# Performance work log

Measured on AMD Instinct MI355X. Metric: run time of the kernel, lower is better.

Reference implementation:

```python
import jax, jax.numpy as jnp
import numpy as np

B, NS, NC = 4096, 1024, 256
GUMBEL_HARD = True


def _linear(x, W, b):
    # torch nn.Linear: y = x @ W.T + b, W is [out, in]
    return x @ W.T + b


def _gumbel_softmax(logits, gnoise, tau, hard):
    y = jax.nn.softmax((logits + gnoise) / tau, axis=-1)
    if hard:
        y_hard = jax.nn.one_hot(jnp.argmax(y, axis=-1), y.shape[-1], dtype=y.dtype)
        y = y_hard + y - jax.lax.stop_gradient(y)  # straight-through
    return y


def setup_inputs() -> dict:
    key = jax.random.key(0)
    ks = jax.random.split(key, 32)
    inp = {
        "ct": jax.random.normal(ks[0], (B, NC), jnp.float32),
        "b1": jax.random.uniform(ks[1], (B, 2), jnp.float32),
        "b2": jax.random.uniform(ks[2], (B, 2), jnp.float32),
        "b3": jax.random.uniform(ks[3], (B, 2), jnp.float32),
        "rnn1": jax.random.normal(ks[4], (B, NS), jnp.float32),
        "rnn2": jax.random.normal(ks[5], (B, NS), jnp.float32),
        "rnn3": jax.random.normal(ks[6], (B, NS), jnp.float32),
        "rnn4": jax.random.normal(ks[7], (B, NS), jnp.float32),
        "gn1": jax.random.gumbel(ks[8], (B, 2), jnp.float32),
        "gn2": jax.random.gumbel(ks[9], (B, 2), jnp.float32),
        "gn3": jax.random.gumbel(ks[10], (B, 2), jnp.float32),
        "theta": 1,
    }
    def lin(k, out_d, in_d):
        return (0.02 * jax.random.normal(k, (out_d, in_d), jnp.float32),
                jnp.zeros((out_d,), jnp.float32))
    shapes = {
        "e_ct": (NS, NC), "rnn1_b0": (NS, 2 * NS), "rnn1_b1": (NS, 2 * NS),
        "b1_rnn1": (2, NS), "rnn2_b0": (NS, 2 * NS), "rnn2_b1": (NS, 2 * NS),
        "b2_rnn2": (2, NS), "rnn3_b0": (NS, 2 * NS), "rnn3_b1": (NS, 2 * NS),
        "b3_rnn3": (2, NS), "rnn4": (NS, 2 * NS), "hg_rnns": (NS, 4 * NS),
        "g_hg": (4, NS), "hctpi_rnns": (NS, 4 * NS), "ctpi_hctpi": (NC, NS),
    }
    for i, (name, (o, ii)) in enumerate(shapes.items()):
        W, bb = lin(ks[11 + i], o, ii)
        inp["W_" + name] = W
        inp["b_" + name] = bb
    return inp


def reference(ct, b1, b2, b3, rnn1, rnn2, rnn3, rnn4, gn1, gn2, gn3, theta,
              W_e_ct, b_e_ct, W_rnn1_b0, b_rnn1_b0, W_rnn1_b1, b_rnn1_b1,
              W_b1_rnn1, b_b1_rnn1, W_rnn2_b0, b_rnn2_b0, W_rnn2_b1, b_rnn2_b1,
              W_b2_rnn2, b_b2_rnn2, W_rnn3_b0, b_rnn3_b0, W_rnn3_b1, b_rnn3_b1,
              W_b3_rnn3, b_b3_rnn3, W_rnn4, b_rnn4, W_hg_rnns, b_hg_rnns,
              W_g_hg, b_g_hg, W_hctpi_rnns, b_hctpi_rnns, W_ctpi_hctpi, b_ctpi_hctpi):
    tau = jnp.float32(theta)
    b1tm1f = b1[:, 0:1]
    ct_e = jax.nn.relu(_linear(ct, W_e_ct, b_e_ct))

    rnn1b1 = jnp.tanh(_linear(jnp.concatenate((rnn2, ct_e), axis=1), W_rnn1_b1, b_rnn1_b1))
    rnn1b0 = jnp.tanh(_linear(jnp.concatenate((rnn1, ct_e), axis=1), W_rnn1_b0, b_rnn1_b0))
    rnn1t = b1tm1f * rnn1b1 + (1.0 - b1tm1f) * rnn1b0
    b1t = _gumbel_softmax(_linear(rnn1t, W_b1_rnn1, b_b1_rnn1), gn1, tau, GUMBEL_HARD)
    b1tf = b1t[:, 0:1]

    b2tm1f = b2[:, 0:1]
    rnn2b1 = jnp.tanh(_linear(jnp.concatenate((rnn3, rnn1t), axis=1), W_rnn2_b1, b_rnn2_b1))
    rnn2b0 = jnp.tanh(_linear(jnp.concatenate((rnn2, rnn1t), axis=1), W_rnn2_b0, b_rnn2_b0))
    rnn2_inner = (1.0 - b2tm1f) * rnn2b0 + b2tm1f * rnn2b1
    rnn2t = (1.0 - b1tf) * rnn2 + b1tf * rnn2_inner
    b2tnew = _gumbel_softmax(_linear(rnn2t, W_b2_rnn2, b_b2_rnn2), gn2, tau, GUMBEL_HARD)
    b2t = b1tf * b2tnew + (1.0 - b1tf) * b2
    b2tf = b2t[:, 0:1]

    b3tm1f = b3[:, 0:1]
    rnn3b1 = jnp.tanh(_linear(jnp.concatenate((rnn4, rnn2t), axis=1), W_rnn3_b1, b_rnn3_b1))
    rnn3b0 = jnp.tanh(_linear(jnp.concatenate((rnn3, rnn2t), axis=1), W_rnn3_b0, b_rnn3_b0))
    rnn3_inner = b3tm1f * rnn3b1 + (1.0 - b3tm1f) * rnn3b0
    rnn3t = (1.0 - b1tf) * rnn3 + b1tf * ((1.0 - b2tf) * rnn3 + b2tf * rnn3_inner)
    b3tnew = _gumbel_softmax(_linear(rnn3t, W_b3_rnn3, b_b3_rnn3), gn3, tau, GUMBEL_HARD)
    b3t = b1tf * (b2tf * b3tnew + (1.0 - b2tf) * b3) + (1.0 - b1tf) * b3
    b3tf = b3t[:, 0:1]

    rnn4_inner = jnp.tanh(_linear(jnp.concatenate((rnn4, rnn3t), axis=1), W_rnn4, b_rnn4))
    rnn4t = (1.0 - b1tf) * rnn4 + b1tf * ((1.0 - b2tf) * rnn4 + b2tf * ((1.0 - b3tf) * rnn4 + b3tf * rnn4_inner))

    hg = jax.nn.relu(_linear(jnp.concatenate((rnn1t, rnn2t, rnn3t, rnn4t), axis=1), W_hg_rnns, b_hg_rnns))
    g = jax.nn.sigmoid(_linear(hg, W_g_hg, b_g_hg))
    gated = jnp.concatenate((g[:, 0:1] * rnn1t, g[:, 1:2] * rnn2t, g[:, 2:3] * rnn3t, g[:, 3:4] * rnn4t), axis=1)
    hctpi = jax.nn.relu(_linear(gated, W_hctpi_rnns, b_hctpi_rnns))
    ctpi = jax.nn.log_softmax(_linear(hctpi, W_ctpi_hctpi, b_ctpi_hctpi), axis=1)
    return (ctpi, b1t, b2t, b3t, rnn1t, rnn2t, rnn3t, rnn4t)
```

## Files before the change

### kernel.cpp

```cpp
#include <hip/hip_runtime.h>
#include <cstdint>
#include <cstddef>

typedef unsigned short u16;
typedef __bf16 bf16x8 __attribute__((ext_vector_type(8)));
typedef float  f32x4  __attribute__((ext_vector_type(4)));
typedef u16    u16x4  __attribute__((ext_vector_type(4)));

__device__ __forceinline__ void splitv(const float4 a, const float4 b, bf16x8& h, bf16x8& l) {
    float x[8] = {a.x, a.y, a.z, a.w, b.x, b.y, b.z, b.w};
#pragma unroll
    for (int i = 0; i < 8; i++) {
        __bf16 hh = (__bf16)x[i];
        h[i] = hh;
        l[i] = (__bf16)(x[i] - (float)hh);
    }
}
__device__ __forceinline__ void hiv(const float4 a, const float4 b, bf16x8& h) {
    float x[8] = {a.x, a.y, a.z, a.w, b.x, b.y, b.z, b.w};
#pragma unroll
    for (int i = 0; i < 8; i++) h[i] = (__bf16)x[i];
}

__device__ __forceinline__ void gl16(const void* g, void* l) {
    __builtin_amdgcn_global_load_lds((__attribute__((address_space(1))) void*)g,
                                     (__attribute__((address_space(3))) void*)l, 16, 0, 0);
}

struct Sec {
    const void* h;
    const u16*  l;
    int lda; int mode;
};
struct GemmArgs {
    Sec A0[4]; Sec A1[4];
    const u16* B0h; const u16* B0l;
    const u16* B1h; const u16* B1l;
    const float* bias0; const float* bias1;
    float* Z0; float* Z1;
    u16* Zh0; u16* Zl0; u16* Zh1; u16* Zl1;
    int bk[4];
    int nsec, ldb, N, spsl, relu, npass, zmode;
};

__global__ __launch_bounds__(256, 4) void gemm_v3(GemmArgs p) {
    __shared__ __align__(16) u16 Ah[128 * 32];
    __shared__ __align__(16) u16 Al[128 * 32];
    __shared__ __align__(16) u16 Bh[64 * 32];
    __shared__ __align__(16) u16 Bl[64 * 32];
    const int tid = threadIdx.x;
    const int lin = blockIdx.x;
    const int mt = ((lin & 7) << 2) | ((lin >> 3) & 3);
    const int nt = lin >> 5;
    const int NTh = p.N >> 6;
    const int half = (nt >= NTh) ? 1 : 0;
    const int n0 = (nt - (half ? NTh : 0)) * 64;
    const int m0 = mt * 128;
    const u16* Bwh = half ? p.B1h : p.B0h;
    const u16* Bwl = half ? p.B1l : p.B0l;
    const float* bia = half ? p.bias1 : p.bias0;
    float* Z = half ? p.Z1 : p.Z0;
    u16* Zh = half ? p.Zh1 : p.Zh0;
    u16* Zl = half ? p.Zl1 : p.Zl0;
    const Sec* As = half ? p.A1 : p.A0;

    const int wave = tid >> 6, lane = tid & 63;
    const int quad = lane >> 4, lr = lane & 15;
    const int wm = (wave & 1) * 64, wn = (wave >> 1) * 32;
    const bool np3 = (p.npass == 3);

    f32x4 acc[4][2];
#pragma unroll
    for (int i = 0; i < 4; i++)
#pragma unroll
        for (int j = 0; j < 2; j++) acc[i][j] = (f32x4){0.f, 0.f, 0.f, 0.f};

    const int arow = tid >> 2;
    const int aslot = tid & 3;
    const int csw = aslot ^ ((arow ^ (arow >> 2)) & 3);
    const int wr_i0 = arow * 32 + csw * 8;
    char* AhB = (char*)Ah; char* AlB = (char*)Al;
    char* BhB = (char*)Bh; char* BlB = (char*)Bl;
    const int ldsw = wave * 1024;

    const int qx8 = ((quad ^ ((lr ^ (lr >> 2)) & 3)) & 3) * 8;

    const int sps = 1 << p.spsl;
    const int total = p.nsec << p.spsl;

    float4 v0a{}, v0b{}, v1a{}, v1b{};
    {
        const Sec s0 = As[0];
        if (s0.mode == 0) {
            const float* a0 = (const float*)s0.h + (size_t)(m0 + arow) * s0.lda + aslot * 8;
            v0a = ((const float4*)a0)[0]; v0b = ((const float4*)a0)[1];
            const float* a1 = a0 + (size_t)64 * s0.lda;
            v1a = ((const float4*)a1)[0]; v1b = ((const float4*)a1)[1];
        }
    }

    for (int tt = 0; tt < total; ++tt) {
        const int s = tt >> p.spsl, t = tt & (sps - 1);
        __syncthreads();
        {
            const size_t off = (size_t)(n0 + arow) * p.ldb + p.bk[s] + t * 32 + csw * 8;
            gl16(Bwh + off, BhB + ldsw);
            if (np3) gl16(Bwl + off, BlB + ldsw);
        }
        const Sec sec = As[s];
        if (sec.mode == 0) {
            if (np3) {
                bf16x8 h, l;
                splitv(v0a, v0b, h, l);
                *(bf16x8*)&Ah[wr_i0] = h;        *(bf16x8*)&Al[wr_i0] = l;
                splitv(v1a, v1b, h, l);
                *(bf16x8*)&Ah[2048 + wr_i0] = h; *(bf16x8*)&Al[2048 + wr_i0] = l;
            } else {
                bf16x8 h;
                hiv(v0a, v0b, h); *(bf16x8*)&Ah[wr_i0] = h;
                hiv(v1a, v1b, h); *(bf16x8*)&Ah[2048 + wr_i0] = h;
            }
        } else {
            const u16* gh = (const u16*)sec.h;
            const size_t o0 = (size_t)(m0 + arow) * sec.lda + t * 32 + csw * 8;
            const size_t o1 = o0 + (size_t)64 * sec.lda;
            gl16(gh + o0, AhB + ldsw);
            gl16(gh + o1, AhB + 4096 + ldsw);
            if (np3) {
                gl16(sec.l + o0, AlB + ldsw);
                gl16(sec.l + o1, AlB + 4096 + ldsw);
            }
        }
        __syncthreads();
        if (tt + 1 < total) {
            const int s2 = (tt + 1) >> p.spsl, t2 = (tt + 1) & (sps - 1);
            const Sec sn = As[s2];
            if (sn.mode == 0) {
                const float* a0 = (const float*)sn.h + (size_t)(m0 + arow) * sn.lda + t2 * 32 + aslot * 8;
                v0a = ((const float4*)a0)[0]; v0b = ((const float4*)a0)[1];
                const float* a1 = a0 + (size_t)64 * sn.lda;
                v1a = ((const float4*)a1)[0]; v1b = ((const float4*)a1)[1];
            }
        }
        bf16x8 ah[4], bh2[2];
#pragma unroll
        for (int i = 0; i < 4; i++)
            ah[i] = *reinterpret_cast<const bf16x8*>(&Ah[(wm + i * 16 + lr) * 32 + qx8]);
#pragma unroll
        for (int j = 0; j < 2; j++)
            bh2[j] = *reinterpret_cast<const bf16x8*>(&Bh[(wn + j * 16 + lr) * 32 + qx8]);
#pragma unroll
        for (int i = 0; i < 4; i++)
#pragma unroll
            for (int j = 0; j < 2; j++)
                acc[i][j] = __builtin_amdgcn_mfma_f32_16x16x32_bf16(ah[i], bh2[j], acc[i][j], 0, 0, 0);
        if (np3) {
            bf16x8 al[4], bl2[2];
#pragma unroll
            for (int i = 0; i < 4; i++)
                al[i] = *reinterpret_cast<const bf16x8*>(&Al[(wm + i * 16 + lr) * 32 + qx8]);
#pragma unroll
            for (int j = 0; j < 2; j++)
                bl2[j] = *reinterpret_cast<const bf16x8*>(&Bl[(wn + j * 16 + lr) * 32 + qx8]);
#pragma unroll
            for (int i = 0; i < 4; i++)
#pragma unroll
                for (int j = 0; j < 2; j++) {
                    acc[i][j] = __builtin_amdgcn_mfma_f32_16x16x32_bf16(ah[i], bl2[j], acc[i][j], 0, 0, 0);
                    acc[i][j] = __builtin_amdgcn_mfma_f32_16x16x32_bf16(al[i], bh2[j], acc[i][j], 0, 0, 0);
                }
        }
    }

#pragma unroll
    for (int j = 0; j < 2; j++) {
        const int n = n0 + wn + j * 16 + lr;
        const float bj = bia[n];
#pragma unroll
        for (int i = 0; i < 4; i++)
#pragma unroll
            for (int r = 0; r < 4; r++) {
                const int m = m0 + wm + i * 16 + quad * 4 + r;
                float v = acc[i][j][r] + bj;
                if (p.relu) v = fmaxf(v, 0.f);
                const size_t zi = (size_t)m * p.N + n;
                if (p.zmode == 0) {
                    Z[zi] = v;
                } else {
                    __bf16 hb = (__bf16)v;
                    Zh[zi] = __builtin_bit_cast(u16, hb);
                    if (p.zmode == 2)
                        Zl[zi] = __builtin_bit_cast(u16, (__bf16)(v - (float)hb));
                }
            }
    }
}

__global__ __launch_bounds__(256) void conv_split(const float* x0, u16* h0, u16* l0, int n0v,
                                                  const float* x1, u16* h1, u16* l1, int n1v) {
    int i = blockIdx.x * 256 + threadIdx.x;
    const float* x; u16* h; u16* l;
    if (i < n0v) { x = x0; h = h0; l = l0; }
    else { i -= n0v; if (i >= n1v) return; x = x1; h = h1; l = l1; }
    const float4 a = ((const float4*)x)[2 * i], b = ((const float4*)x)[2 * i + 1];
    bf16x8 hh, ll;
    if (l) { splitv(a, b, hh, ll); ((bf16x8*)h)[i] = hh; ((bf16x8*)l)[i] = ll; }
    else   { hiv(a, b, hh);        ((bf16x8*)h)[i] = hh; }
}

__device__ __forceinline__ void store_hl4(const float4 o, u16* hp, u16* lp, int base) {
    float xs[4] = {o.x, o.y, o.z, o.w};
    u16x4 hv, lv;
#pragma unroll
    for (int k = 0; k < 4; k++) {
        __bf16 hb = (__bf16)xs[k];
        hv[k] = __builtin_bit_cast(u16, hb);
        if (lp) lv[k] = __builtin_bit_cast(u16, (__bf16)(xs[k] - (float)hb));
    }
    *(u16x4*)(hp + base) = hv;
    if (lp) *(u16x4*)(lp + base) = lv;
}

__global__ __launch_bounds__(256) void combine1(const float* Z0, const float* Z1, const float* b1in,
                                                float* outr, u16* hO, u16* lO) {
    const int base = (blockIdx.x * 256 + threadIdx.x) * 4;
    const int m = base >> 10;
    const float bf = b1in[2 * m];
    const float4 z0 = *(const float4*)(Z0 + base), z1 = *(const float4*)(Z1 + base);
    float4 o;
    o.x = bf * tanhf(z1.x) + (1.f - bf) * tanhf(z0.x);
    o.y = bf * tanhf(z1.y) + (1.f - bf) * tanhf(z0.y);
    o.z = bf * tanhf(z1.z) + (1.f - bf) * tanhf(z0.z);
    o.w = bf * tanhf(z1.w) + (1.f - bf) * tanhf(z0.w);
    *(float4*)(outr + base) = o;
    store_hl4(o, hO, lO, base);
}
__global__ __launch_bounds__(256) void combine2(const float* Z0, const float* Z1, const float* b2in,
                                                const float* rnn2in, const float* F1, float* outr,
                                                u16* hO, u16* lO) {
    const int base = (blockIdx.x * 256 + threadIdx.x) * 4;
    const int m = base >> 10;
    const float b2f = b2in[2 * m], f1 = F1[m];
    const float4 z0 = *(const float4*)(Z0 + base), z1 = *(const float4*)(Z1 + base);
    const float4 r2 = *(const float4*)(rnn2in + base);
    float4 o;
    o.x = (1.f - f1) * r2.x + f1 * ((1.f - b2f) * tanhf(z0.x) + b2f * tanhf(z1.x));
    o.y = (1.f - f1) * r2.y + f1 * ((1.f - b2f) * tanhf(z0.y) + b2f * tanhf(z1.y));
    o.z = (1.f - f1) * r2.z + f1 * ((1.f - b2f) * tanhf(z0.z) + b2f * tanhf(z1.z));
    o.w = (1.f - f1) * r2.w + f1 * ((1.f - b2f) * tanhf(z0.w) + b2f * tanhf(z1.w));
    *(float4*)(outr + base) = o;
    store_hl4(o, hO, lO, base);
}
__global__ __launch_bounds__(256) void combine3(const float* Z0, const float* Z1, const float* b3in,
                                                const float* rnn3in, const float* F1, const float* F2,
                                                float* outr, u16* hO) {
    const int base = (blockIdx.x * 256 + threadIdx.x) * 4;
    const int m = base >> 10;
    const float b3f = b3in[2 * m], f1 = F1[m], f2 = F2[m];
    const float4 z0 = *(const float4*)(Z0 + base), z1 = *(const float4*)(Z1 + base);
    const float4 r3 = *(const float4*)(rnn3in + base);
    float4 o;
    o.x = (1.f - f1) * r3.x + f1 * ((1.f - f2) * r3.x + f2 * (b3f * tanhf(z1.x) + (1.f - b3f) * tanhf(z0.x)));
    o.y = (1.f - f1) * r3.y + f1 * ((1.f - f2) * r3.y + f2 * (b3f * tanhf(z1.y) + (1.f - b3f) * tanhf(z0.y)));
    o.z = (1.f - f1) * r3.z + f1 * ((1.f - f2) * r3.z + f2 * (b3f * tanhf(z1.z) + (1.f - b3f) * tanhf(z0.z)));
    o.w = (1.f - f1) * r3.w + f1 * ((1.f - f2) * r3.w + f2 * (b3f * tanhf(z1.w) + (1.f - b3f) * tanhf(z0.w)));
    *(float4*)(outr + base) = o;
    store_hl4(o, hO, nullptr, base);
}
__global__ __launch_bounds__(256) void combine4(const float* Z0, const float* rnn4in, const float* F1,
                                                const float* F2, const float* F3, float* outr, u16* hO) {
    const int base = (blockIdx.x * 256 + threadIdx.x) * 4;
    const int m = base >> 10;
    const float f1 = F1[m], f2 = F2[m], f3 = F3[m];
    const float4 z0 = *(const float4*)(Z0 + base);
    const float4 r4 = *(const float4*)(rnn4in + base);
    float4 o;
    o.x = (1.f - f1) * r4.x + f1 * ((1.f - f2) * r4.x + f2 * ((1.f - f3) * r4.x + f3 * tanhf(z0.x)));
    o.y = (1.f - f1) * r4.y + f1 * ((1.f - f2) * r4.y + f2 * ((1.f - f3) * r4.y + f3 * tanhf(z0.y)));
    o.z = (1.f - f1) * r4.z + f1 * ((1.f - f2) * r4.z + f2 * ((1.f - f3) * r4.z + f3 * tanhf(z0.z)));
    o.w = (1.f - f1) * r4.w + f1 * ((1.f - f2) * r4.w + f2 * ((1.f - f3) * r4.w + f3 * tanhf(z0.w)));
    *(float4*)(outr + base) = o;
    store_hl4(o, hO, nullptr, base);
}

__global__ __launch_bounds__(256) void gemv_decide(const float* x, const float* W2, const float* bias2,
                                                   const float* gn, const float* bprev,
                                                   const float* Fp1, const float* Fp2,
                                                   float* bout, float* fout, int stage) {
    const int wave = threadIdx.x >> 6, lane = threadIdx.x & 63;
    const int m = blockIdx.x * 4 + wave;
    const float* row = x + (size_t)m * 1024;
    float s0 = 0.f, s1 = 0.f;
#pragma unroll 4
    for (int i = 0; i < 16; i++) {
        const int k = lane + 64 * i;
        const float v = row[k];
        s0 += v * W2[k];
        s1 += v * W2[1024 + k];
    }
    for (int off = 32; off > 0; off >>= 1) { s0 += __shfl_xor(s0, off); s1 += __shfl_xor(s1, off); }
    if (lane == 0) {
        const float l0 = s0 + bias2[0] + gn[2 * m];
        const float l1 = s1 + bias2[1] + gn[2 * m + 1];
        const float nf = (l0 >= l1) ? 1.f : 0.f;
        float v0, v1;
        if (stage == 1) {
            v0 = nf; v1 = 1.f - nf;
        } else if (stage == 2) {
            const float f1 = Fp1[m];
            const float p0 = bprev[2 * m], p1 = bprev[2 * m + 1];
            v0 = f1 * nf + (1.f - f1) * p0;
            v1 = f1 * (1.f - nf) + (1.f - f1) * p1;
        } else {
            const float f1 = Fp1[m], f2 = Fp2[m];
            const float p0 = bprev[2 * m], p1 = bprev[2 * m + 1];
            const float i0 = f2 * nf + (1.f - f2) * p0;
            const float i1 = f2 * (1.f - nf) + (1.f - f2) * p1;
            v0 = f1 * i0 + (1.f - f1) * p0;
            v1 = f1 * i1 + (1.f - f1) * p1;
        }
        fout[m] = v0;
        bout[2 * m] = v0; bout[2 * m + 1] = v1;
    }
}

__global__ __launch_bounds__(256) void gemv_g4(const float* hg, const float* Wg, const float* bg, float* G) {
    const int wave = threadIdx.x >> 6, lane = threadIdx.x & 63;
    const int m = blockIdx.x * 4 + wave;
    const float* row = hg + (size_t)m * 1024;
    float s[4] = {0.f, 0.f, 0.f, 0.f};
#pragma unroll 4
    for (int i = 0; i < 16; i++) {
        const int k = lane + 64 * i;
        const float v = row[k];
#pragma unroll
        for (int j = 0; j < 4; j++) s[j] += v * Wg[j * 1024 + k];
    }
    for (int off = 32; off > 0; off >>= 1)
#pragma unroll
        for (int j = 0; j < 4; j++) s[j] += __shfl_xor(s[j], off);
    if (lane == 0) {
#pragma unroll
        for (int j = 0; j < 4; j++) G[m * 4 + j] = 1.f / (1.f + expf(-(s[j] + bg[j])));
    }
}

__global__ __launch_bounds__(256) void gated_k(const float* rnnF, const float* G, u16* gatedh) {
    const int base = (blockIdx.x * 256 + threadIdx.x) * 4;
    const int m = base >> 12, rem = base & 4095;
    const int j = rem >> 10, k = rem & 1023;
    const float g = G[m * 4 + j];
    const float4 r = *(const float4*)(rnnF + (size_t)j * 4194304 + (size_t)m * 1024 + k);
    u16x4 hv;
    hv[0] = __builtin_bit_cast(u16, (__bf16)(g * r.x));
    hv[1] = __builtin_bit_cast(u16, (__bf16)(g * r.y));
    hv[2] = __builtin_bit_cast(u16, (__bf16)(g * r.z));
    hv[3] = __builtin_bit_cast(u16, (__bf16)(g * r.w));
    *(u16x4*)(gatedh + base) = hv;
}

__global__ __launch_bounds__(256) void logsoftmax_k(const float* Z, float* out) {
    const int wave = threadIdx.x >> 6, lane = threadIdx.x & 63;
    const int row = blockIdx.x * 4 + wave;
    const size_t base = (size_t)row * 256;
    float x[4];
#pragma unroll
    for (int i = 0; i < 4; i++) x[i] = Z[base + lane + 64 * i];
    float mx = fmaxf(fmaxf(x[0], x[1]), fmaxf(x[2], x[3]));
    for (int off = 32; off > 0; off >>= 1) mx = fmaxf(mx, __shfl_xor(mx, off));
    float s = 0.f;
#pragma unroll
    for (int i = 0; i < 4; i++) s += expf(x[i] - mx);
    for (int off = 32; off > 0; off >>= 1) s += __shfl_xor(s, off);
    const float lse = mx + logf(s);
#pragma unroll
    for (int i = 0; i < 4; i++) out[base + lane + 64 * i] = x[i] - lse;
}

static const size_t OUT_B1 = 1048576, OUT_B2 = 1056768, OUT_B3 = 1064960;
static const size_t OUT_R1 = 1073152, OUT_R2 = 5267456, OUT_R3 = 9461760, OUT_R4 = 13656064;

static inline Sec S0(const float* f, int lda) { Sec s; s.h = f; s.l = nullptr; s.lda = lda; s.mode = 0; return s; }
static inline Sec S1(const u16* h, const u16* l, int lda) { Sec s; s.h = h; s.l = l; s.lda = lda; s.mode = 1; return s; }

extern "C" void kernel_launch(void* const* d_in, const int* in_sizes, int n_in,
                              void* d_out, int out_size, void* d_ws, size_t ws_size,
                              hipStream_t stream) {
    (void)in_sizes; (void)n_in; (void)out_size; (void)ws_size;
    const float* ct   = (const float*)d_in[0];
    const float* b1   = (const float*)d_in[1];
    const float* b2   = (const float*)d_in[2];
    const float* b3   = (const float*)d_in[3];
    const float* rnn1 = (const float*)d_in[4];
    const float* rnn2 = (const float*)d_in[5];
    const float* rnn3 = (const float*)d_in[6];
    const float* rnn4 = (const float*)d_in[7];
    const float* gn1  = (const float*)d_in[8];
    const float* gn2  = (const float*)d_in[9];
    const float* gn3  = (const float*)d_in[10];
    const float* W_e    = (const float*)d_in[12]; const float* be    = (const float*)d_in[13];
    const float* W_r1b0 = (const float*)d_in[14]; const float* br1b0 = (const float*)d_in[15];
    const float* W_r1b1 = (const float*)d_in[16]; const float* br1b1 = (const float*)d_in[17];
    const float* W_b1   = (const float*)d_in[18]; const float* bb1   = (const float*)d_in[19];
    const float* W_r2b0 = (const float*)d_in[20]; const float* br2b0 = (const float*)d_in[21];
    const float* W_r2b1 = (const float*)d_in[22]; const float* br2b1 = (const float*)d_in[23];
    const float* W_b2   = (const float*)d_in[24]; const float* bb2   = (const float*)d_in[25];
    const float* W_r3b0 = (const float*)d_in[26]; const float* br3b0 = (const float*)d_in[27];
    const float* W_r3b1 = (const float*)d_in[28]; const float* br3b1 = (const float*)d_in[29];
    const float* W_b3   = (const float*)d_in[30]; const float* bb3   = (const float*)d_in[31];
    const float* W_r4   = (const float*)d_in[32]; const float* br4   = (const float*)d_in[33];
    const float* W_hg   = (const float*)d_in[34]; const float* bhg   = (const float*)d_in[35];
    const float* W_g    = (const float*)d_in[36]; const float* bg    = (const float*)d_in[37];
    const float* W_hct  = (const float*)d_in[38]; const float* bhct  = (const float*)d_in[39];
    const float* W_ct   = (const float*)d_in[40]; const float* bct   = (const float*)d_in[41];

    float* out = (float*)d_out;
    char* w = (char*)d_ws;
    const size_t MB = 1024 * 1024;
    float* Z0    = (float*)(w);
    float* Z1    = (float*)(w + 16 * MB);
    u16* WS      = (u16*)(w + 32 * MB);
    u16* CTEFh   = (u16*)(w + 48 * MB);
    u16* CTEFl   = (u16*)(w + 56 * MB);
    u16* R1h     = (u16*)(w + 64 * MB);
    u16* R1l     = (u16*)(w + 72 * MB);
    u16* R2h     = (u16*)(w + 48 * MB);
    u16* R2l     = (u16*)(w + 56 * MB);
    u16* R3h     = (u16*)(w + 72 * MB);
    u16* R4h     = (u16*)(w + 56 * MB);
    float* HGF   = (float*)(w);
    u16* GATEDh  = (u16*)(w);
    u16* HCTFh   = (u16*)(w + 48 * MB);
    float* ZC    = (float*)(w);
    float* F1 = out; float* F2 = F1 + 4096; float* F3 = F1 + 8192; float* G4 = F1 + 12288;
    float* R1 = out + OUT_R1; float* R2 = out + OUT_R2;
    float* R3 = out + OUT_R3; float* R4 = out + OUT_R4;

    const int NWe = 32768, NWr = 262144, NWg = 524288, NWct = 32768;
    auto conv = [&](const float* x0, u16* h0, u16* l0, int n0v,
                    const float* x1, u16* h1, u16* l1, int n1v) {
        const int tot = n0v + n1v;
        conv_split<<<dim3((tot + 255) / 256), 256, 0, stream>>>(x0, h0, l0, n0v, x1, h1, l1, n1v);
    };
    const dim3 EW(4096), GV(1024);

    conv(W_e, WS, WS + 262144, NWe, nullptr, nullptr, nullptr, 0);
    {
        GemmArgs p{};
        p.A0[0] = S0(ct, 256); p.A1[0] = p.A0[0];
        p.B0h = WS; p.B0l = WS + 262144; p.B1h = p.B0h; p.B1l = p.B0l;
        p.bias0 = be; p.bias1 = be;
        p.Zh0 = CTEFh; p.Zl0 = CTEFl; p.Zh1 = CTEFh; p.Zl1 = CTEFl;
        p.bk[0] = 0; p.nsec = 1; p.ldb = 256; p.N = 1024; p.spsl = 3;
        p.relu = 1; p.npass = 3; p.zmode = 2;
        gemm_v3<<<dim3(16 * 32), 256, 0, stream>>>(p);
    }
    conv(W_r1b0, WS, WS + 2097152, NWr, W_r1b1, WS + 4194304, WS + 6291456, NWr);
    {
        GemmArgs p{};
        p.A0[0] = S0(rnn1, 1024); p.A0[1] = S1(CTEFh, CTEFl, 1024);
        p.A1[0] = S0(rnn2, 1024); p.A1[1] = p.A0[1];
        p.B0h = WS; p.B0l = WS + 2097152; p.B1h = WS + 4194304; p.B1l = WS + 6291456;
        p.bias0 = br1b0; p.bias1 = br1b1;
        p.Z0 = Z0; p.Z1 = Z1;
        p.bk[0] = 0; p.bk[1] = 1024; p.nsec = 2; p.ldb = 2048; p.N = 1024; p.spsl = 5;
        p.relu = 0; p.npass = 3; p.zmode = 0;
        gemm_v3<<<dim3(32 * 32), 256, 0, stream>>>(p);
    }
    combine1<<<EW, 256, 0, stream>>>(Z0, Z1, b1, R1, R1h, R1l);
    gemv_decide<<<GV, 256, 0, stream>>>(R1, W_b1, bb1, gn1, b1, F1, F1, out + OUT_B1, F1, 1);
    conv(W_r2b0, WS, WS + 2097152, NWr, W_r2b1, WS + 4194304, WS + 6291456, NWr);
    {
        GemmArgs p{};
        p.A0[0] = S0(rnn2, 1024); p.A0[1] = S1(R1h, R1l, 1024);
        p.A1[0] = S0(rnn3, 1024); p.A1[1] = p.A0[1];
        p.B0h = WS; p.B0l = WS + 2097152; p.B1h = WS + 4194304; p.B1l = WS + 6291456;
        p.bias0 = br2b0; p.bias1 = br2b1;
        p.Z0 = Z0; p.Z1 = Z1;
        p.bk[0] = 0; p.bk[1] = 1024; p.nsec = 2; p.ldb = 2048; p.N = 1024; p.spsl = 5;
        p.relu = 0; p.npass = 3; p.zmode = 0;
        gemm_v3<<<dim3(32 * 32), 256, 0, stream>>>(p);
    }
    combine2<<<EW, 256, 0, stream>>>(Z0, Z1, b2, rnn2, F1, R2, R2h, R2l);
    gemv_decide<<<GV, 256, 0, stream>>>(R2, W_b2, bb2, gn2, b2, F1, F1, out + OUT_B2, F2, 2);
    conv(W_r3b0, WS, WS + 2097152, NWr, W_r3b1, WS + 4194304, WS + 6291456, NWr);
    {
        GemmArgs p{};
        p.A0[0] = S0(rnn3, 1024); p.A0[1] = S1(R2h, R2l, 1024);
        p.A1[0] = S0(rnn4, 1024); p.A1[1] = p.A0[1];
        p.B0h = WS; p.B0l = WS + 2097152; p.B1h = WS + 4194304; p.B1l = WS + 6291456;
        p.bias0 = br3b0; p.bias1 = br3b1;
        p.Z0 = Z0; p.Z1 = Z1;
        p.bk[0] = 0; p.bk[1] = 1024; p.nsec = 2; p.ldb = 2048; p.N = 1024; p.spsl = 5;
        p.relu = 0; p.npass = 3; p.zmode = 0;
        gemm_v3<<<dim3(32 * 32), 256, 0, stream>>>(p);
    }
    combine3<<<EW, 256, 0, stream>>>(Z0, Z1, b3, rnn3, F1, F2, R3, R3h);
    gemv_decide<<<GV, 256, 0, stream>>>(R3, W_b3, bb3, gn3, b3, F1, F2, out + OUT_B3, F3, 3);
    conv(W_r4, WS, nullptr, NWr, nullptr, nullptr, nullptr, 0);
    {
        GemmArgs p{};
        p.A0[0] = S0(rnn4, 1024); p.A0[1] = S1(R3h, nullptr, 1024);
        p.A1[0] = p.A0[0]; p.A1[1] = p.A0[1];
        p.B0h = WS; p.B0l = nullptr; p.B1h = WS; p.B1l = nullptr;
        p.bias0 = br4; p.bias1 = br4;
        p.Z0 = Z0; p.Z1 = Z0;
        p.bk[0] = 0; p.bk[1] = 1024; p.nsec = 2; p.ldb = 2048; p.N = 1024; p.spsl = 5;
        p.relu = 0; p.npass = 1; p.zmode = 0;
        gemm_v3<<<dim3(16 * 32), 256, 0, stream>>>(p);
    }
    combine4<<<EW, 256, 0, stream>>>(Z0, rnn4, F1, F2, F3, R4, R4h);
    conv(W_hg, WS, nullptr, NWg, nullptr, nullptr, nullptr, 0);
    {
        GemmArgs p{};
        p.A0[0] = S1(R1h, nullptr, 1024); p.A0[1] = S1(R2h, nullptr, 1024);
        p.A0[2] = S1(R3h, nullptr, 1024); p.A0[3] = S1(R4h, nullptr, 1024);
        p.A1[0] = p.A0[0]; p.A1[1] = p.A0[1]; p.A1[2] = p.A0[2]; p.A1[3] = p.A0[3];
        p.B0h = WS; p.B1h = WS;
        p.bias0 = bhg; p.bias1 = bhg;
        p.Z0 = HGF; p.Z1 = HGF;
        p.bk[0] = 0; p.bk[1] = 1024; p.bk[2] = 2048; p.bk[3] = 3072;
        p.nsec = 4; p.ldb = 4096; p.N = 1024; p.spsl = 5;
        p.relu = 1; p.npass = 1; p.zmode = 0;
        gemm_v3<<<dim3(16 * 32), 256, 0, stream>>>(p);
    }
    gemv_g4<<<GV, 256, 0, stream>>>(HGF, W_g, bg, G4);
    gated_k<<<dim3(16384), 256, 0, stream>>>(R1, G4, GATEDh);
    conv(W_hct, WS, nullptr, NWg, nullptr, nullptr, nullptr, 0);
    {
        GemmArgs p{};
        p.A0[0] = S1(GATEDh, nullptr, 4096); p.A1[0] = p.A0[0];
        p.B0h = WS; p.B1h = WS;
        p.bias0 = bhct; p.bias1 = bhct;
        p.Zh0 = HCTFh; p.Zh1 = HCTFh;
        p.bk[0] = 0; p.nsec = 1; p.ldb = 4096; p.N = 1024; p.spsl = 7;
        p.relu = 1; p.npass = 1; p.zmode = 1;
        gemm_v3<<<dim3(16 * 32), 256, 0, stream>>>(p);
    }
    conv(W_ct, WS, nullptr, NWct, nullptr, nullptr, nullptr, 0);
    {
        GemmArgs p{};
        p.A0[0] = S1(HCTFh, nullptr, 1024); p.A1[0] = p.A0[0];
        p.B0h = WS; p.B1h = WS;
        p.bias0 = bct; p.bias1 = bct;
        p.Z0 = ZC; p.Z1 = ZC;
        p.bk[0] = 0; p.nsec = 1; p.ldb = 1024; p.N = 256; p.spsl = 5;
        p.relu = 0; p.npass = 1; p.zmode = 0;
        gemm_v3<<<dim3(4 * 32), 256, 0, stream>>>(p);
    }
    logsoftmax_k<<<GV, 256, 0, stream>>>(ZC, out);
}
```

Measured before the change: 946.7 us.

## Double-buffer GEMM LDS tiles and template on pass count

Converts the GEMM main loop to double-buffered LDS, staging the next K-tile (async global-to-LDS loads plus the fp32-to-bf16 split writes) while MFMAs run on the current tile. Each iteration now needs one barrier instead of two, with explicit waitcnt control and raised wave priority around the MFMA block. The kernel is templated on the 1-pass vs 3-pass split, so the unused low-part paths and buffers are compiled out. LDS use doubles, and the 3-pass variant lowers its launch bound to 3 blocks per CU, which can reduce occupancy.

```diff
diff --git a/kernel.cpp b/kernel.cpp
--- a/kernel.cpp
+++ b/kernel.cpp
@@ -40,14 +40,17 @@
     float* Z0; float* Z1;
     u16* Zh0; u16* Zl0; u16* Zh1; u16* Zl1;
     int bk[4];
-    int nsec, ldb, N, spsl, relu, npass, zmode;
+    int nsec, ldb, N, spsl, relu, zmode;
 };
 
-__global__ __launch_bounds__(256, 4) void gemm_v3(GemmArgs p) {
-    __shared__ __align__(16) u16 Ah[128 * 32];
-    __shared__ __align__(16) u16 Al[128 * 32];
-    __shared__ __align__(16) u16 Bh[64 * 32];
-    __shared__ __align__(16) u16 Bl[64 * 32];
+template <int NP>
+__global__ __launch_bounds__(256, NP == 3 ? 3 : 4) void gemm_v4(GemmArgs p) {
+    constexpr bool NP3 = (NP == 3);
+    __shared__ __align__(16) u16 AhS[2][4096];
+    __shared__ __align__(16) u16 BhS[2][2048];
+    __shared__ __align__(16) u16 AlS[NP3 ? 2 : 1][NP3 ? 4096 : 8];
+    __shared__ __align__(16) u16 BlS[NP3 ? 2 : 1][NP3 ? 2048 : 8];
+
     const int tid = threadIdx.x;
     const int lin = blockIdx.x;
     const int mt = ((lin & 7) << 2) | ((lin >> 3) & 3);
@@ -67,7 +70,6 @@
     const int wave = tid >> 6, lane = tid & 63;
     const int quad = lane >> 4, lr = lane & 15;
     const int wm = (wave & 1) * 64, wn = (wave >> 1) * 32;
-    const bool np3 = (p.npass == 3);
 
     f32x4 acc[4][2];
 #pragma unroll
@@ -79,89 +81,102 @@
     const int aslot = tid & 3;
     const int csw = aslot ^ ((arow ^ (arow >> 2)) & 3);
     const int wr_i0 = arow * 32 + csw * 8;
-    char* AhB = (char*)Ah; char* AlB = (char*)Al;
-    char* BhB = (char*)Bh; char* BlB = (char*)Bl;
     const int ldsw = wave * 1024;
-
     const int qx8 = ((quad ^ ((lr ^ (lr >> 2)) & 3)) & 3) * 8;
 
     const int sps = 1 << p.spsl;
     const int total = p.nsec << p.spsl;
 
     float4 v0a{}, v0b{}, v1a{}, v1b{};
+
+    auto regload = [&](const Sec& sec, int t) {
+        const float* a0 = (const float*)sec.h + (size_t)(m0 + arow) * sec.lda + t * 32 + aslot * 8;
+        v0a = ((const float4*)a0)[0]; v0b = ((const float4*)a0)[1];
+        const float* a1 = a0 + (size_t)64 * sec.lda;
+        v1a = ((const float4*)a1)[0]; v1b = ((const float4*)a1)[1];
+    };
+    auto writeA0 = [&](int buf) {
+        if constexpr (NP3) {
+            bf16x8 h, l;
+            splitv(v0a, v0b, h, l);
+            *(bf16x8*)&AhS[buf][wr_i0] = h;        *(bf16x8*)&AlS[buf][wr_i0] = l;
+            splitv(v1a, v1b, h, l);
+            *(bf16x8*)&AhS[buf][2048 + wr_i0] = h; *(bf16x8*)&AlS[buf][2048 + wr_i0] = l;
+        } else {
+            bf16x8 h;
+            hiv(v0a, v0b, h); *(bf16x8*)&AhS[buf][wr_i0] = h;
+            hiv(v1a, v1b, h); *(bf16x8*)&AhS[buf][2048 + wr_i0] = h;
+        }
+    };
+    auto stageA1 = [&](int buf, const Sec& sec, int t) {
+        const u16* gh = (const u16*)sec.h;
+        const size_t o0 = (size_t)(m0 + arow) * sec.lda + t * 32 + csw * 8;
+        const size_t o1 = o0 + (size_t)64 * sec.lda;
+        gl16(gh + o0, (char*)&AhS[buf][0] + ldsw);
+        gl16(gh + o1, (char*)&AhS[buf][0] + 4096 + ldsw);
+        if constexpr (NP3) {
+            gl16(sec.l + o0, (char*)&AlS[buf][0] + ldsw);
+            gl16(sec.l + o1, (char*)&AlS[buf][0] + 4096 + ldsw);
+        }
+    };
+    auto stageB = [&](int buf, int s, int t) {
+        const size_t off = (size_t)(n0 + arow) * p.ldb + p.bk[s] + t * 32 + csw * 8;
+        gl16(Bwh + off, (char*)&BhS[buf][0] + ldsw);
+        if constexpr (NP3) gl16(Bwl + off, (char*)&BlS[buf][0] + ldsw);
+    };
+
+    stageB(0, 0, 0);
     {
         const Sec s0 = As[0];
-        if (s0.mode == 0) {
-            const float* a0 = (const float*)s0.h + (size_t)(m0 + arow) * s0.lda + aslot * 8;
-            v0a = ((const float4*)a0)[0]; v0b = ((const float4*)a0)[1];
-            const float* a1 = a0 + (size_t)64 * s0.lda;
-            v1a = ((const float4*)a1)[0]; v1b = ((const float4*)a1)[1];
-        }
-    }
+        if (s0.mode == 0) { regload(s0, 0); writeA0(0); }
+        else stageA1(0, s0, 0);
+    }
+    if (total > 1) {
+        const Sec s1 = As[1 >> p.spsl];
+        if (s1.mode == 0) regload(s1, 1 & (sps - 1));
+    }
+    asm volatile("s_waitcnt vmcnt(0) lgkmcnt(0)" ::: "memory");
+    __builtin_amdgcn_s_barrier();
+    __builtin_amdgcn_sched_barrier(0);
 
     for (int tt = 0; tt < total; ++tt) {
-        const int s = tt >> p.spsl, t = tt & (sps - 1);
-        __syncthreads();
-        {
-            const size_t off = (size_t)(n0 + arow) * p.ldb + p.bk[s] + t * 32 + csw * 8;
-            gl16(Bwh + off, BhB + ldsw);
-            if (np3) gl16(Bwl + off, BlB + ldsw);
-        }
-        const Sec sec = As[s];
-        if (sec.mode == 0) {
-            if (np3) {
-                bf16x8 h, l;
-                splitv(v0a, v0b, h, l);
-                *(bf16x8*)&Ah[wr_i0] = h;        *(bf16x8*)&Al[wr_i0] = l;
-                splitv(v1a, v1b, h, l);
-                *(bf16x8*)&Ah[2048 + wr_i0] = h; *(bf16x8*)&Al[2048 + wr_i0] = l;
-            } else {
-                bf16x8 h;
-                hiv(v0a, v0b, h); *(bf16x8*)&Ah[wr_i0] = h;
-                hiv(v1a, v1b, h); *(bf16x8*)&Ah[2048 + wr_i0] = h;
+        const int cur = tt & 1, nxt = cur ^ 1;
+        bool rl = false;
+        if (tt + 1 < total) {
+            const int u = tt + 1, s = u >> p.spsl, t = u & (sps - 1);
+            stageB(nxt, s, t);
+            const Sec sec = As[s];
+            if (sec.mode == 0) writeA0(nxt);
+            else stageA1(nxt, sec, t);
+            __builtin_amdgcn_sched_barrier(0);
+            if (tt + 2 < total) {
+                const int s2 = (tt + 2) >> p.spsl;
+                const Sec sec2 = As[s2];
+                if (sec2.mode == 0) { regload(sec2, (tt + 2) & (sps - 1)); rl = true; }
             }
-        } else {
-            const u16* gh = (const u16*)sec.h;
-            const size_t o0 = (size_t)(m0 + arow) * sec.lda + t * 32 + csw * 8;
-            const size_t o1 = o0 + (size_t)64 * sec.lda;
-            gl16(gh + o0, AhB + ldsw);
-            gl16(gh + o1, AhB + 4096 + ldsw);
-            if (np3) {
-                gl16(sec.l + o0, AlB + ldsw);
-                gl16(sec.l + o1, AlB + 4096 + ldsw);
-            }
-        }
-        __syncthreads();
-        if (tt + 1 < total) {
-            const int s2 = (tt + 1) >> p.spsl, t2 = (tt + 1) & (sps - 1);
-            const Sec sn = As[s2];
-            if (sn.mode == 0) {
-                const float* a0 = (const float*)sn.h + (size_t)(m0 + arow) * sn.lda + t2 * 32 + aslot * 8;
-                v0a = ((const float4*)a0)[0]; v0b = ((const float4*)a0)[1];
-                const float* a1 = a0 + (size_t)64 * sn.lda;
-                v1a = ((const float4*)a1)[0]; v1b = ((const float4*)a1)[1];
-            }
+            __builtin_amdgcn_sched_barrier(0);
         }
         bf16x8 ah[4], bh2[2];
 #pragma unroll
         for (int i = 0; i < 4; i++)
-            ah[i] = *reinterpret_cast<const bf16x8*>(&Ah[(wm + i * 16 + lr) * 32 + qx8]);
+            ah[i] = *reinterpret_cast<const bf16x8*>(&AhS[cur][(wm + i * 16 + lr) * 32 + qx8]);
 #pragma unroll
         for (int j = 0; j < 2; j++)
-            bh2[j] = *reinterpret_cast<const bf16x8*>(&Bh[(wn + j * 16 + lr) * 32 + qx8]);
+            bh2[j] = *reinterpret_cast<const bf16x8*>(&BhS[cur][(wn + j * 16 + lr) * 32 + qx8]);
+        __builtin_amdgcn_s_setprio(1);
 #pragma unroll
         for (int i = 0; i < 4; i++)
 #pragma unroll
             for (int j = 0; j < 2; j++)
                 acc[i][j] = __builtin_amdgcn_mfma_f32_16x16x32_bf16(ah[i], bh2[j], acc[i][j], 0, 0, 0);
-        if (np3) {
+        if constexpr (NP3) {
             bf16x8 al[4], bl2[2];
 #pragma unroll
             for (int i = 0; i < 4; i++)
-                al[i] = *reinterpret_cast<const bf16x8*>(&Al[(wm + i * 16 + lr) * 32 + qx8]);
+                al[i] = *reinterpret_cast<const bf16x8*>(&AlS[cur][(wm + i * 16 + lr) * 32 + qx8]);
 #pragma unroll
             for (int j = 0; j < 2; j++)
-                bl2[j] = *reinterpret_cast<const bf16x8*>(&Bl[(wn + j * 16 + lr) * 32 + qx8]);
+                bl2[j] = *reinterpret_cast<const bf16x8*>(&BlS[cur][(wn + j * 16 + lr) * 32 + qx8]);
 #pragma unroll
             for (int i = 0; i < 4; i++)
 #pragma unroll
@@ -170,6 +185,11 @@
                     acc[i][j] = __builtin_amdgcn_mfma_f32_16x16x32_bf16(al[i], bh2[j], acc[i][j], 0, 0, 0);
                 }
         }
+        __builtin_amdgcn_s_setprio(0);
+        if (rl) asm volatile("s_waitcnt vmcnt(4) lgkmcnt(0)" ::: "memory");
+        else    asm volatile("s_waitcnt vmcnt(0) lgkmcnt(0)" ::: "memory");
+        __builtin_amdgcn_s_barrier();
+        __builtin_amdgcn_sched_barrier(0);
     }
 
 #pragma unroll
@@ -442,6 +462,10 @@
         const int tot = n0v + n1v;
         conv_split<<<dim3((tot + 255) / 256), 256, 0, stream>>>(x0, h0, l0, n0v, x1, h1, l1, n1v);
     };
+    auto launch = [&](const GemmArgs& p, int NT, int npass) {
+        if (npass == 3) gemm_v4<3><<<dim3(NT * 32), 256, 0, stream>>>(p);
+        else            gemm_v4<1><<<dim3(NT * 32), 256, 0, stream>>>(p);
+    };
     const dim3 EW(4096), GV(1024);
 
     conv(W_e, WS, WS + 262144, NWe, nullptr, nullptr, nullptr, 0);
@@ -452,8 +476,8 @@
         p.bias0 = be; p.bias1 = be;
         p.Zh0 = CTEFh; p.Zl0 = CTEFl; p.Zh1 = CTEFh; p.Zl1 = CTEFl;
         p.bk[0] = 0; p.nsec = 1; p.ldb = 256; p.N = 1024; p.spsl = 3;
-        p.relu = 1; p.npass = 3; p.zmode = 2;
-        gemm_v3<<<dim3(16 * 32), 256, 0, stream>>>(p);
+        p.relu = 1; p.zmode = 2;
+        launch(p, 16, 3);
     }
     conv(W_r1b0, WS, WS + 2097152, NWr, W_r1b1, WS + 4194304, WS + 6291456, NWr);
     {
@@ -464,8 +488,8 @@
         p.bias0 = br1b0; p.bias1 = br1b1;
         p.Z0 = Z0; p.Z1 = Z1;
         p.bk[0] = 0; p.bk[1] = 1024; p.nsec = 2; p.ldb = 2048; p.N = 1024; p.spsl = 5;
-        p.relu = 0; p.npass = 3; p.zmode = 0;
-        gemm_v3<<<dim3(32 * 32), 256, 0, stream>>>(p);
+        p.relu = 0; p.zmode = 0;
+        launch(p, 32, 3);
     }
     combine1<<<EW, 256, 0, stream>>>(Z0, Z1, b1, R1, R1h, R1l);
     gemv_decide<<<GV, 256, 0, stream>>>(R1, W_b1, bb1, gn1, b1, F1, F1, out + OUT_B1, F1, 1);
@@ -478,8 +502,8 @@
         p.bias0 = br2b0; p.bias1 = br2b1;
         p.Z0 = Z0; p.Z1 = Z1;
         p.bk[0] = 0; p.bk[1] = 1024; p.nsec = 2; p.ldb = 2048; p.N = 1024; p.spsl = 5;
-        p.relu = 0; p.npass = 3; p.zmode = 0;
-        gemm_v3<<<dim3(32 * 32), 256, 0, stream>>>(p);
+        p.relu = 0; p.zmode = 0;
+        launch(p, 32, 3);
     }
     combine2<<<EW, 256, 0, stream>>>(Z0, Z1, b2, rnn2, F1, R2, R2h, R2l);
     gemv_decide<<<GV, 256, 0, stream>>>(R2, W_b2, bb2, gn2, b2, F1, F1, out + OUT_B2, F2, 2);
@@ -492,8 +516,8 @@
         p.bias0 = br3b0; p.bias1 = br3b1;
         p.Z0 = Z0; p.Z1 = Z1;
         p.bk[0] = 0; p.bk[1] = 1024; p.nsec = 2; p.ldb = 2048; p.N = 1024; p.spsl = 5;
-        p.relu = 0; p.npass = 3; p.zmode = 0;
-        gemm_v3<<<dim3(32 * 32), 256, 0, stream>>>(p);
+        p.relu = 0; p.zmode = 0;
+        launch(p, 32, 3);
     }
     combine3<<<EW, 256, 0, stream>>>(Z0, Z1, b3, rnn3, F1, F2, R3, R3h);
     gemv_decide<<<GV, 256, 0, stream>>>(R3, W_b3, bb3, gn3, b3, F1, F2, out + OUT_B3, F3, 3);
@@ -506,8 +530,8 @@
         p.bias0 = br4; p.bias1 = br4;
         p.Z0 = Z0; p.Z1 = Z0;
         p.bk[0] = 0; p.bk[1] = 1024; p.nsec = 2; p.ldb = 2048; p.N = 1024; p.spsl = 5;
-        p.relu = 0; p.npass = 1; p.zmode = 0;
-        gemm_v3<<<dim3(16 * 32), 256, 0, stream>>>(p);
+        p.relu = 0; p.zmode = 0;
+        launch(p, 16, 1);
     }
     combine4<<<EW, 256, 0, stream>>>(Z0, rnn4, F1, F2, F3, R4, R4h);
     conv(W_hg, WS, nullptr, NWg, nullptr, nullptr, nullptr, 0);
@@ -521,8 +545,8 @@
         p.Z0 = HGF; p.Z1 = HGF;
         p.bk[0] = 0; p.bk[1] = 1024; p.bk[2] = 2048; p.bk[3] = 3072;
         p.nsec = 4; p.ldb = 4096; p.N = 1024; p.spsl = 5;
-        p.relu = 1; p.npass = 1; p.zmode = 0;
-        gemm_v3<<<dim3(16 * 32), 256, 0, stream>>>(p);
+        p.relu = 1; p.zmode = 0;
+        launch(p, 16, 1);
     }
     gemv_g4<<<GV, 256, 0, stream>>>(HGF, W_g, bg, G4);
     gated_k<<<dim3(16384), 256, 0, stream>>>(R1, G4, GATEDh);
@@ -534,8 +558,8 @@
         p.bias0 = bhct; p.bias1 = bhct;
         p.Zh0 = HCTFh; p.Zh1 = HCTFh;
         p.bk[0] = 0; p.nsec = 1; p.ldb = 4096; p.N = 1024; p.spsl = 7;
-        p.relu = 1; p.npass = 1; p.zmode = 1;
-        gemm_v3<<<dim3(16 * 32), 256, 0, stream>>>(p);
+        p.relu = 1; p.zmode = 1;
+        launch(p, 16, 1);
     }
     conv(W_ct, WS, nullptr, NWct, nullptr, nullptr, nullptr, 0);
     {
@@ -545,8 +569,8 @@
         p.bias0 = bct; p.bias1 = bct;
         p.Z0 = ZC; p.Z1 = ZC;
         p.bk[0] = 0; p.nsec = 1; p.ldb = 1024; p.N = 256; p.spsl = 5;
-        p.relu = 0; p.npass = 1; p.zmode = 0;
-        gemm_v3<<<dim3(4 * 32), 256, 0, stream>>>(p);
+        p.relu = 0; p.zmode = 0;
+        launch(p, 4, 1);
     }
     logsoftmax_k<<<GV, 256, 0, stream>>>(ZC, out);
 }
```

After: 1.058 ms. 11.8% more time.
